# Optimization experiments

Hardware: AMD Instinct MI355X
Metric: run time of the kernel (lower is better)

## Reference

```python
import jax, jax.numpy as jnp
import numpy as np

N, DEG = 20000, 16
E = N * DEG
D_IN, D_HID, D_OUT, L = 1024, 512, 128, 3


def setup_inputs() -> dict:
    key = jax.random.key(0)
    ks = jax.random.split(key, 16)
    scale = 0.02
    X = jax.random.normal(ks[0], (N, D_IN), dtype=jnp.float32)
    senders = jax.random.randint(ks[1], (E,), 0, N)
    receivers = jnp.repeat(jnp.arange(N), DEG)  # sorted, every node has DEG neighbors
    inp = {"X": X, "senders": senders, "receivers": receivers}
    ki = 2
    for l in range(L):
        din = D_IN >> l
        dh = D_HID >> l
        inp[f"lw{l}"] = jax.random.normal(ks[ki], (2 * din, dh), jnp.float32) * scale; ki += 1
        inp[f"lb{l}"] = jnp.zeros((dh,), jnp.float32)
        inp[f"aw{l}"] = jax.random.normal(ks[ki], (din, dh), jnp.float32) * scale; ki += 1
        inp[f"aq{l}"] = jax.random.normal(ks[ki], (dh,), jnp.float32) * scale; ki += 1
    inp["ow"] = jax.random.normal(ks[ki], (D_HID >> (L - 1), D_OUT), jnp.float32) * scale
    inp["ob"] = jnp.zeros((D_OUT,), jnp.float32)
    return inp


def _attend(h, senders, receivers, aw, aq):
    # scores depend only on the neighbor (sender) embedding: q @ relu(W h_j)
    logits = jnp.einsum('nh,h->n', jax.nn.relu(h @ aw), aq)            # [N]
    el = logits[senders]                                               # [E]
    m = jax.ops.segment_max(el, receivers, num_segments=N)            # per-receiver max
    w = jnp.exp(el - m[receivers])                                     # [E]
    denom = jax.ops.segment_sum(w, receivers, num_segments=N)         # [N]
    msg = jax.ops.segment_sum(w[:, None] * h[senders], receivers, num_segments=N)  # [N,D]
    return msg / denom[:, None]


def reference(X, senders, receivers,
              lw0, lb0, aw0, aq0,
              lw1, lb1, aw1, aq1,
              lw2, lb2, aw2, aq2,
              ow, ob):
    params = [(lw0, lb0, aw0, aq0), (lw1, lb1, aw1, aq1), (lw2, lb2, aw2, aq2)]
    h = X
    for lw, lb, aw, aq in params:
        hN = _attend(h, senders, receivers, aw, aq)
        h = jax.nn.relu(jnp.concatenate([h, hN], axis=1) @ lw + lb)
    return h[14] @ ow + ob
```

## Files before the change

### kernel.cpp

```cpp
#include <hip/hip_runtime.h>
#include <math.h>

typedef unsigned short ushort_t;
typedef __attribute__((ext_vector_type(8))) short short8;
typedef __attribute__((ext_vector_type(4))) float f32x4;

#define NN    20000
#define DEG   16
constexpr int MAXL2 = 17;
constexpr int MAXL1 = 289;
constexpr int L0PAD = 73 * 64;

__device__ __forceinline__ ushort_t f2bf(float f) {
    unsigned u = __float_as_uint(f);
    return (ushort_t)((u + 0x7FFFu + ((u >> 16) & 1u)) >> 16);
}

__global__ __launch_bounds__(256)
void k_frontier(const int* __restrict__ senders,
                int* __restrict__ list2, int* __restrict__ inv2,
                int* __restrict__ list1, int* __restrict__ inv1,
                int* __restrict__ cnts,
                const float* __restrict__ aw0, ushort_t* __restrict__ awT,
                const float* __restrict__ aw1,
                const float* __restrict__ lw1, const float* __restrict__ aw2,
                const float* __restrict__ lw2, const float* __restrict__ ow,
                float* __restrict__ dummy,
                float4* __restrict__ zp, int n4, int nzb) {
    int t = threadIdx.x;
    int bb = (int)blockIdx.x;
    if (bb > 0) {
        int b = bb - 1;
        if (b < nzb) {
            int i = b * 256 + t;
            if (i < n4) zp[i] = make_float4(0.f, 0.f, 0.f, 0.f);
            return;
        }
        b -= nzb;
        if (b < 512) {
            __shared__ float tile[32][33];
            int bx = b & 15, by = b >> 4;
            int i0 = t >> 3, j0 = (t & 7) * 4;
            float4 v = *(const float4*)(aw0 + (size_t)(by * 32 + i0) * 512 + bx * 32 + j0);
            tile[i0][j0] = v.x; tile[i0][j0 + 1] = v.y; tile[i0][j0 + 2] = v.z; tile[i0][j0 + 3] = v.w;
            __syncthreads();
            int n = bx * 32 + i0, kc = j0;
            ushort4 o;
            o.x = f2bf(tile[kc][i0]);     o.y = f2bf(tile[kc + 1][i0]);
            o.z = f2bf(tile[kc + 2][i0]); o.w = f2bf(tile[kc + 3][i0]);
            *(ushort4*)(awT + (size_t)n * 1024 + by * 32 + kc) = o;
            return;
        }
        b -= 512;
        const float4* src; int base;
        if (b < 64)        { src = (const float4*)lw1; base = b * 1024; }
        else if (b < 96)   { src = (const float4*)aw1; base = (b - 64) * 1024; }
        else if (b < 104)  { src = (const float4*)aw2; base = (b - 96) * 1024; }
        else if (b < 120)  { src = (const float4*)lw2; base = (b - 104) * 1024; }
        else               { src = (const float4*)ow;  base = (b - 120) * 1024; }
        float s = 0.f;
#pragma unroll
        for (int i = 0; i < 4; i++) {
            float4 v = src[base + i * 256 + t];
            s += v.x + v.y + v.z + v.w;
        }
        if (s == 1234.5678f) dummy[0] = s;
        return;
    }
    __shared__ unsigned bm[625];
    __shared__ int cnt;
    __shared__ int lloc[MAXL2];
    auto clear = [&]() { for (int i = t; i < 625; i += 256) bm[i] = 0u; if (t == 0) cnt = 0; };
    clear(); __syncthreads();
    if (t < 17) {
        int node = (t < 16) ? senders[14 * DEG + t] : 14;
        unsigned bit = 1u << (node & 31);
        unsigned old = atomicOr(&bm[node >> 5], bit);
        if (!(old & bit)) { int p = atomicAdd(&cnt, 1); list2[p] = node; inv2[node] = p; lloc[p] = node; }
    }
    __syncthreads();
    int c2 = cnt;
    if (t == 0) cnts[2] = c2;
    __syncthreads(); clear(); __syncthreads();
    for (int i = t; i < c2 * 17; i += 256) {
        int r = i / 17, k = i - r * 17;
        int node = (k < 16) ? senders[lloc[r] * DEG + k] : lloc[r];
        unsigned bit = 1u << (node & 31);
        unsigned old = atomicOr(&bm[node >> 5], bit);
        if (!(old & bit)) { int p = atomicAdd(&cnt, 1); list1[p] = node; inv1[node] = p; }
    }
    __syncthreads();
    if (t == 0) { int c1 = cnt; cnts[1] = c1; cnts[0] = c1 * 16; }
}

__global__ __launch_bounds__(256)
void k_prep(const float* __restrict__ X, const int* __restrict__ senders,
            const int* __restrict__ list1, const int* __restrict__ cnts,
            ushort_t* __restrict__ Xg) {
    int r = blockIdx.x;
    int t = threadIdx.x;
    int rc = cnts[0];
    ushort4 o = make_ushort4(0, 0, 0, 0);
    if (r < rc) {
        int n = list1[r >> 4];
        int s = senders[n * DEG + (r & 15)];
        float4 v = *(const float4*)(X + (size_t)s * 1024 + t * 4);
        o.x = f2bf(v.x); o.y = f2bf(v.y); o.z = f2bf(v.z); o.w = f2bf(v.w);
    }
    *(ushort4*)(Xg + (size_t)r * 1024 + t * 4) = o;
}

__global__ __launch_bounds__(256)
void k_logits_mfma(const ushort_t* __restrict__ Xg,
                   const ushort_t* __restrict__ WT,
                   const float* __restrict__ aq, float* __restrict__ lgc,
                   const int* __restrict__ cnt) {
    __shared__ short As[64 * 40];
    __shared__ short Bs[64 * 40];
    int rcnt = *cnt;
    int row0 = blockIdx.x * 64;
    if (row0 >= rcnt) return;
    int col0 = blockIdx.y * 64;
    int t = threadIdx.x;
    int w = t >> 6, lane = t & 63;

    int sr = t >> 2, sk = (t & 3) * 8;
    const ushort_t* ap = Xg + (size_t)(row0 + sr) * 1024 + sk;
    const ushort_t* bp = WT + (size_t)(col0 + sr) * 1024 + sk;

    int fm = lane & 15, fq = lane >> 4;
    const short* arow = As + (w * 16 + fm) * 40 + fq * 8;
    const short* brow = Bs + fm * 40 + fq * 8;

    f32x4 acc0 = {0.f,0.f,0.f,0.f}, acc1 = {0.f,0.f,0.f,0.f};
    f32x4 acc2 = {0.f,0.f,0.f,0.f}, acc3 = {0.f,0.f,0.f,0.f};

    short8 pa = *(const short8*)(ap);
    short8 pb = *(const short8*)(bp);
    for (int k0 = 0; k0 < 1024; k0 += 32) {
        *(short8*)(As + sr * 40 + sk) = pa;
        *(short8*)(Bs + sr * 40 + sk) = pb;
        __syncthreads();
        if (k0 + 32 < 1024) {
            pa = *(const short8*)(ap + k0 + 32);
            pb = *(const short8*)(bp + k0 + 32);
        }
        short8 af = *(const short8*)arow;
        short8 b0 = *(const short8*)(brow);
        short8 b1 = *(const short8*)(brow + 16 * 40);
        short8 b2 = *(const short8*)(brow + 32 * 40);
        short8 b3 = *(const short8*)(brow + 48 * 40);
        acc0 = __builtin_amdgcn_mfma_f32_16x16x32_bf16(af, b0, acc0, 0, 0, 0);
        acc1 = __builtin_amdgcn_mfma_f32_16x16x32_bf16(af, b1, acc1, 0, 0, 0);
        acc2 = __builtin_amdgcn_mfma_f32_16x16x32_bf16(af, b2, acc2, 0, 0, 0);
        acc3 = __builtin_amdgcn_mfma_f32_16x16x32_bf16(af, b3, acc3, 0, 0, 0);
        __syncthreads();
    }

    float aqv0 = aq[col0 + fm],      aqv1 = aq[col0 + 16 + fm];
    float aqv2 = aq[col0 + 32 + fm], aqv3 = aq[col0 + 48 + fm];
#pragma unroll
    for (int r = 0; r < 4; r++) {
        float v = fmaxf(acc0[r], 0.f) * aqv0 + fmaxf(acc1[r], 0.f) * aqv1
                + fmaxf(acc2[r], 0.f) * aqv2 + fmaxf(acc3[r], 0.f) * aqv3;
#pragma unroll
        for (int off = 1; off < 16; off <<= 1) v += __shfl_xor(v, off);
        if (fm == 0) atomicAdd(&lgc[row0 + w * 16 + fq * 4 + r], v);
    }
}

__global__ __launch_bounds__(256)
void k_agg0(const float* __restrict__ X, const float* __restrict__ lgc0,
            const int* __restrict__ senders, const int* __restrict__ list1,
            const int* __restrict__ cnt1, float* __restrict__ hN0) {
    __shared__ int   s_row[DEG];
    __shared__ float s_w[DEG];
    __shared__ float s_sc;
    int b = blockIdx.x;
    if (b >= *cnt1) return;
    int t = threadIdx.x;
    if (t < DEG) {
        s_row[t] = senders[list1[b] * DEG + t];
        s_w[t]   = lgc0[b * DEG + t];
    }
    __syncthreads();
    if (t == 0) {
        float m = -1e30f;
        for (int k = 0; k < DEG; k++) m = fmaxf(m, s_w[k]);
        float d = 0.f;
        for (int k = 0; k < DEG; k++) { float w = __expf(s_w[k] - m); s_w[k] = w; d += w; }
        s_sc = 1.f / d;
    }
    __syncthreads();
    float scale = s_sc;
    int dI = t * 4;
    float4 acc = make_float4(0.f, 0.f, 0.f, 0.f);
#pragma unroll
    for (int k = 0; k < DEG; k++) {
        float w = s_w[k];
        float4 v = *(const float4*)(X + (size_t)s_row[k] * 1024 + dI);
        acc.x += w * v.x; acc.y += w * v.y; acc.z += w * v.z; acc.w += w * v.w;
    }
    acc.x *= scale; acc.y *= scale; acc.z *= scale; acc.w *= scale;
    *(float4*)(hN0 + (size_t)b * 1024 + dI) = acc;
}

__global__ __launch_bounds__(256)
void k_mm0(const float* __restrict__ X, const float* __restrict__ hN0,
           const int* __restrict__ list1, const float* __restrict__ B,
           float* __restrict__ C0p, const int* __restrict__ cnt) {
    __shared__ float As[32][68];
    __shared__ float Bs[32][64];
    int rcnt = *cnt;
    int row0 = blockIdx.x * 64;
    if (row0 >= rcnt) return;
    int col0 = blockIdx.y * 64;
    int kbeg = blockIdx.z * 128;
    int t = threadIdx.x;
    int ty = t >> 4, tx = t & 15;
    int lr = t >> 2, kaoff = (t & 3) * 4;
    int grow = row0 + lr;
    bool rowValid = grow < rcnt;
    const float* rp;
    if (kbeg < 1024) rp = rowValid ? X + (size_t)list1[grow] * 1024 + kbeg : X;
    else             rp = rowValid ? hN0 + (size_t)grow * 1024 + (kbeg - 1024) : hN0;
    const float* Bp = B + (size_t)kbeg * 512 + col0;
    int bidx0 = t, bidx1 = t + 256;

    auto loadA = [&](int k) -> float4 {
        if (!rowValid) return make_float4(0.f, 0.f, 0.f, 0.f);
        return *(const float4*)(rp + k);
    };
    auto loadB = [&](int idx, int k0) -> float4 {
        int row = idx >> 4, c4 = (idx & 15) * 4;
        return *(const float4*)(Bp + (size_t)(k0 + row) * 512 + c4);
    };

    float4 pa0 = loadA(kaoff);
    float4 pa1 = loadA(kaoff + 16);
    float4 pb0 = loadB(bidx0, 0);
    float4 pb1 = loadB(bidx1, 0);

    float acc[4][4] = {};
    for (int k0 = 0; k0 < 128; k0 += 32) {
        As[kaoff + 0][lr] = pa0.x; As[kaoff + 1][lr] = pa0.y;
        As[kaoff + 2][lr] = pa0.z; As[kaoff + 3][lr] = pa0.w;
        As[kaoff + 16][lr] = pa1.x; As[kaoff + 17][lr] = pa1.y;
        As[kaoff + 18][lr] = pa1.z; As[kaoff + 19][lr] = pa1.w;
        *(float4*)&Bs[bidx0 >> 4][(bidx0 & 15) * 4] = pb0;
        *(float4*)&Bs[bidx1 >> 4][(bidx1 & 15) * 4] = pb1;
        __syncthreads();
        if (k0 + 32 < 128) {
            pa0 = loadA(k0 + 32 + kaoff);
            pa1 = loadA(k0 + 32 + kaoff + 16);
            pb0 = loadB(bidx0, k0 + 32);
            pb1 = loadB(bidx1, k0 + 32);
        }
#pragma unroll
        for (int kk = 0; kk < 32; kk++) {
            float4 a4 = *(const float4*)&As[kk][ty * 4];
            float4 b4 = *(const float4*)&Bs[kk][tx * 4];
            float a[4] = {a4.x, a4.y, a4.z, a4.w};
            float b[4] = {b4.x, b4.y, b4.z, b4.w};
#pragma unroll
            for (int i = 0; i < 4; i++)
#pragma unroll
                for (int j = 0; j < 4; j++) acc[i][j] += a[i] * b[j];
        }
        __syncthreads();
    }
#pragma unroll
    for (int i = 0; i < 4; i++) {
        int r = row0 + ty * 4 + i;
        if (r < rcnt) {
            float* Crow = C0p + ((size_t)blockIdx.z * MAXL1 + r) * 512 + col0 + tx * 4;
            *(float4*)Crow = make_float4(acc[i][0], acc[i][1], acc[i][2], acc[i][3]);
        }
    }
}

__global__ __launch_bounds__(256)
void k_bias_logits(const float* __restrict__ C0p, const float* __restrict__ lb0,
                   const float* __restrict__ aw1, const float* __restrict__ aq1,
                   float* __restrict__ h1, float* __restrict__ lgc1,
                   const int* __restrict__ cnt) {
    __shared__ float sh[512];
    __shared__ float red[4];
    int r = blockIdx.x;
    if (r >= *cnt) return;
    int t = threadIdx.x;
    float v0 = lb0[t], v1 = lb0[256 + t];
    const float* base = C0p + (size_t)r * 512;
#pragma unroll
    for (int z = 0; z < 16; z++) {
        v0 += base[(size_t)z * MAXL1 * 512 + t];
        v1 += base[(size_t)z * MAXL1 * 512 + 256 + t];
    }
    v0 = v0 > 0.f ? v0 : 0.f;
    v1 = v1 > 0.f ? v1 : 0.f;
    sh[t] = v0; sh[256 + t] = v1;
    h1[(size_t)r * 512 + t] = v0;
    h1[(size_t)r * 512 + 256 + t] = v1;
    __syncthreads();
    float dot = 0.f;
    for (int k = 0; k < 512; k += 4) {
        dot += sh[k + 0] * aw1[(size_t)(k + 0) * 256 + t]
             + sh[k + 1] * aw1[(size_t)(k + 1) * 256 + t]
             + sh[k + 2] * aw1[(size_t)(k + 2) * 256 + t]
             + sh[k + 3] * aw1[(size_t)(k + 3) * 256 + t];
    }
    float v = (dot > 0.f ? dot : 0.f) * aq1[t];
#pragma unroll
    for (int off = 1; off < 64; off <<= 1) v += __shfl_xor(v, off);
    if ((t & 63) == 0) red[t >> 6] = v;
    __syncthreads();
    if (t == 0) lgc1[r] = red[0] + red[1] + red[2] + red[3];
}

__global__ __launch_bounds__(256)
void k_tail1(const float* __restrict__ h1, const float* __restrict__ lgc1,
             const int* __restrict__ senders, const int* __restrict__ list2,
             const int* __restrict__ inv1, const int* __restrict__ cnts,
             const float* __restrict__ lw1, const float* __restrict__ lb1,
             float* __restrict__ h2) {
    __shared__ __align__(16) float As[17][1024];
    __shared__ float sw[17][16];
    __shared__ int   srow[17][16];
    __shared__ int   orow[17];
    __shared__ float psum[16][17 * 16];
    int c2 = cnts[2];
    int t = threadIdx.x;
    int b = blockIdx.x;

    for (int i = t; i < c2 * 16; i += 256) {
        int j = i >> 4, k = i & 15;
        int s = senders[list2[j] * DEG + k];
        int rr = inv1[s];
        srow[j][k] = rr;
        sw[j][k] = lgc1[rr];
    }
    if (t < c2) orow[t] = inv1[list2[t]];
    __syncthreads();
    if (t < c2) {
        float m = -1e30f;
        for (int k = 0; k < 16; k++) m = fmaxf(m, sw[t][k]);
        float d = 0.f;
        for (int k = 0; k < 16; k++) { float w = __expf(sw[t][k] - m); sw[t][k] = w; d += w; }
        float inv = 1.f / d;
        for (int k = 0; k < 16; k++) sw[t][k] *= inv;
    }
    __syncthreads();
    for (int e = t; e < c2 * 128; e += 256) {
        int j = e >> 7, d4 = (e & 127) * 4;
        *(float4*)&As[j][d4] = *(const float4*)&h1[(size_t)orow[j] * 512 + d4];
        float4 a = make_float4(0.f, 0.f, 0.f, 0.f);
#pragma unroll
        for (int k = 0; k < 16; k++) {
            float w = sw[j][k];
            float4 v = *(const float4*)&h1[(size_t)srow[j][k] * 512 + d4];
            a.x += w * v.x; a.y += w * v.y; a.z += w * v.z; a.w += w * v.w;
        }
        *(float4*)&As[j][512 + d4] = a;
    }
    __syncthreads();
    int c = t & 15, s = t >> 4;
    int gc = b * 16 + c;
    float acc[17];
#pragma unroll
    for (int j = 0; j < 17; j++) acc[j] = 0.f;
    for (int k = s * 64; k < s * 64 + 64; k += 4) {
        float b0 = lw1[(size_t)(k + 0) * 256 + gc];
        float b1 = lw1[(size_t)(k + 1) * 256 + gc];
        float b2 = lw1[(size_t)(k + 2) * 256 + gc];
        float b3 = lw1[(size_t)(k + 3) * 256 + gc];
#pragma unroll
        for (int j = 0; j < 17; j++) {
            float4 a = *(const float4*)&As[j][k];
            acc[j] += a.x * b0 + a.y * b1 + a.z * b2 + a.w * b3;
        }
    }
#pragma unroll
    for (int j = 0; j < 17; j++) psum[s][j * 16 + c] = acc[j];
    __syncthreads();
    for (int e = t; e < c2 * 16; e += 256) {
        int j = e >> 4, cc = e & 15;
        float v = 0.f;
#pragma unroll
        for (int s2 = 0; s2 < 16; s2++) v += psum[s2][j * 16 + cc];
        v += lb1[b * 16 + cc];
        h2[(size_t)j * 256 + b * 16 + cc] = v > 0.f ? v : 0.f;
    }
}

__global__ __launch_bounds__(512)
void k_tail2(const float* __restrict__ h2, const int* __restrict__ senders,
             const int* __restrict__ inv2, const int* __restrict__ cnts,
             const float* __restrict__ aw2, const float* __restrict__ aq2,
             const float* __restrict__ lw2, const float* __restrict__ lb2,
             const float* __restrict__ ow, const float* __restrict__ ob,
             float* __restrict__ out) {
    __shared__ __align__(16) float sh2[17][256];
    __shared__ __align__(16) float psum[8][17][128];
    __shared__ __align__(16) float h3in[512];
    __shared__ __align__(16) float sh3[128];
    __shared__ __align__(16) float psumB[16][128];
    __shared__ float slog[17];
    __shared__ float swt[16];
    __shared__ int   srow2[16];
    __shared__ int   srow14;
    int c2 = cnts[2];
    int t = threadIdx.x;
    for (int e = t; e < c2 * 64; e += 512) {
        int j = e >> 6, d4 = (e & 63) * 4;
        *(float4*)&sh2[j][d4] = *(const float4*)&h2[(size_t)j * 256 + d4];
    }
    if (t < c2) slog[t] = 0.f;
    if (t < 16) srow2[t] = inv2[senders[14 * DEG + t]];
    if (t == 31) srow14 = inv2[14];
    __syncthreads();
    {
        int cg = t & 31;
        int s  = (t >> 5) & 7;
        int jg = t >> 8;
        int j0 = jg * 9;
        int jend = min(c2, j0 + 9);
        float4 acc[9];
#pragma unroll
        for (int i = 0; i < 9; i++) acc[i] = make_float4(0.f, 0.f, 0.f, 0.f);
        const float* ap = aw2 + cg * 4;
        for (int k = s * 32; k < s * 32 + 32; k++) {
            float4 bv = *(const float4*)(ap + (size_t)k * 128);
#pragma unroll
            for (int i = 0; i < 9; i++) {
                int j = j0 + i;
                if (j < jend) {
                    float a = sh2[j][k];
                    acc[i].x += a * bv.x; acc[i].y += a * bv.y;
                    acc[i].z += a * bv.z; acc[i].w += a * bv.w;
                }
            }
        }
#pragma unroll
        for (int i = 0; i < 9; i++) {
            int j = j0 + i;
            if (j < jend) *(float4*)&psum[s][j][cg * 4] = acc[i];
        }
    }
    __syncthreads();
    for (int e = t; e < c2 * 128; e += 512) {
        int j = e >> 7, c = e & 127;
        float v = 0.f;
#pragma unroll
        for (int s = 0; s < 8; s++) v += psum[s][j][c];
        v = v > 0.f ? v : 0.f;
        atomicAdd(&slog[j], v * aq2[c]);
    }
    __syncthreads();
    if (t == 0) {
        float m = -1e30f;
        for (int k = 0; k < 16; k++) m = fmaxf(m, slog[srow2[k]]);
        float d = 0.f;
        for (int k = 0; k < 16; k++) { float w = __expf(slog[srow2[k]] - m); swt[k] = w; d += w; }
        float inv = 1.f / d;
        for (int k = 0; k < 16; k++) swt[k] *= inv;
    }
    __syncthreads();
    if (t < 256) {
        float a = 0.f;
#pragma unroll
        for (int k = 0; k < 16; k++) a += swt[k] * sh2[srow2[k]][t];
        h3in[256 + t] = a;
    } else {
        int d = t - 256;
        h3in[d] = sh2[srow14][d];
    }
    __syncthreads();
    {
        int cg = t & 31, s = t >> 5;
        float4 acc = make_float4(0.f, 0.f, 0.f, 0.f);
        const float* bp = lw2 + cg * 4;
        for (int k = s * 32; k < s * 32 + 32; k++) {
            float4 bv = *(const float4*)(bp + (size_t)k * 128);
            float a = h3in[k];
            acc.x += a * bv.x; acc.y += a * bv.y; acc.z += a * bv.z; acc.w += a * bv.w;
        }
        *(float4*)&psumB[s][cg * 4] = acc;
    }
    __syncthreads();
    if (t < 128) {
        float v = lb2[t];
#pragma unroll
        for (int s = 0; s < 16; s++) v += psumB[s][t];
        sh3[t] = v > 0.f ? v : 0.f;
    }
    __syncthreads();
    {
        int cg = t & 31, s = t >> 5;
        float4 acc = make_float4(0.f, 0.f, 0.f, 0.f);
        const float* bp = ow + cg * 4;
        for (int k = s * 8; k < s * 8 + 8; k++) {
            float4 bv = *(const float4*)(bp + (size_t)k * 128);
            float a = sh3[k];
            acc.x += a * bv.x; acc.y += a * bv.y; acc.z += a * bv.z; acc.w += a * bv.w;
        }
        *(float4*)&psumB[s][cg * 4] = acc;
    }
    __syncthreads();
    if (t < 128) {
        float v = ob[t];
#pragma unroll
        for (int s = 0; s < 16; s++) v += psumB[s][t];
        out[t] = v;
    }
}

extern "C" void kernel_launch(void* const* d_in, const int* in_sizes, int n_in,
                              void* d_out, int out_size, void* d_ws, size_t ws_size,
                              hipStream_t stream) {
    const float* X       = (const float*)d_in[0];
    const int*   senders = (const int*)d_in[1];
    const float* lw0 = (const float*)d_in[3];
    const float* lb0 = (const float*)d_in[4];
    const float* aw0 = (const float*)d_in[5];
    const float* aq0 = (const float*)d_in[6];
    const float* lw1 = (const float*)d_in[7];
    const float* lb1 = (const float*)d_in[8];
    const float* aw1 = (const float*)d_in[9];
    const float* aq1 = (const float*)d_in[10];
    const float* lw2 = (const float*)d_in[11];
    const float* lb2 = (const float*)d_in[12];
    const float* aw2 = (const float*)d_in[13];
    const float* aq2 = (const float*)d_in[14];
    const float* owp = (const float*)d_in[15];
    const float* obp = (const float*)d_in[16];
    float* out = (float*)d_out;

    char* ws = (char*)d_ws;
    size_t off = 0;
    auto alloc = [&](size_t nbytes) -> void* {
        void* p = ws + off;
        off += (nbytes + 255) & ~(size_t)255;
        return p;
    };
    float* lgc0 = (float*)alloc(L0PAD * 4);
    size_t zero_end = off;
    float* lgc1 = (float*)alloc(MAXL1 * 4);
    int* inv1  = (int*)alloc(NN * 4);
    int* inv2  = (int*)alloc(NN * 4);
    int* list1 = (int*)alloc(MAXL1 * 4);
    int* list2 = (int*)alloc(MAXL2 * 4);
    int* cnts  = (int*)alloc(16);
    float* dummy = (float*)alloc(16);
    ushort_t* Xg  = (ushort_t*)alloc((size_t)L0PAD * 1024 * 2);
    ushort_t* awT = (ushort_t*)alloc((size_t)512 * 1024 * 2);
    float* C0p  = (float*)alloc((size_t)16 * MAXL1 * 512 * 4);
    float* hN0c = (float*)alloc((size_t)MAXL1 * 1024 * 4);
    float* h1c  = (float*)alloc((size_t)MAXL1 * 512 * 4);
    float* h2c  = (float*)alloc((size_t)MAXL2 * 256 * 4);
    (void)in_sizes; (void)n_in; (void)out_size; (void)ws_size;

    int nz4 = (int)(zero_end / 16);
    int nzb = (nz4 + 255) / 256;

    hipLaunchKernelGGL(k_frontier, dim3(1 + nzb + 512 + 124), dim3(256), 0, stream,
                       senders, list2, inv2, list1, inv1, cnts,
                       aw0, awT, aw1, lw1, aw2, lw2, owp, dummy,
                       (float4*)ws, nz4, nzb);
    hipLaunchKernelGGL(k_prep, dim3(L0PAD), dim3(256), 0, stream,
                       X, senders, list1, cnts, Xg);
    hipLaunchKernelGGL(k_logits_mfma, dim3(73, 8), dim3(256), 0, stream,
                       Xg, awT, aq0, lgc0, cnts + 0);
    hipLaunchKernelGGL(k_agg0, dim3(MAXL1), dim3(256), 0, stream,
                       X, lgc0, senders, list1, cnts + 1, hN0c);
    hipLaunchKernelGGL(k_mm0, dim3(5, 8, 16), dim3(256), 0, stream,
                       X, hN0c, list1, lw0, C0p, cnts + 1);
    hipLaunchKernelGGL(k_bias_logits, dim3(MAXL1), dim3(256), 0, stream,
                       C0p, lb0, aw1, aq1, h1c, lgc1, cnts + 1);
    hipLaunchKernelGGL(k_tail1, dim3(16), dim3(256), 0, stream,
                       h1c, lgc1, senders, list2, inv1, cnts, lw1, lb1, h2c);
    hipLaunchKernelGGL(k_tail2, dim3(1), dim3(512), 0, stream,
                       h2c, senders, inv2, cnts, aw2, aq2, lw2, lb2, owp, obp, out);
}
```

Before: 246.9 us.

## Fuse layer-0 aggregation into logits kernel and drop frontier deduplication

The layer-0 softmax aggregation kernel is folded into the MFMA logits kernel. A per-row-panel atomic counter lets the last of the 8 column blocks for a panel run aggregation for its 4 nodes, which removes one kernel launch. The layer-1 frontier is no longer deduplicated with a bitmap. It now lists every sender slot directly (c2*17 entries), so duplicate nodes get recomputed and inv1 is overwritten by the last writer. This skips a sync and the atomics, but the redundant rows add extra work downstream and the ordering of inv1 changes.

```diff
diff --git a/kernel.cpp b/kernel.cpp
--- a/kernel.cpp
+++ b/kernel.cpp
@@ -70,8 +70,9 @@
     __shared__ unsigned bm[625];
     __shared__ int cnt;
     __shared__ int lloc[MAXL2];
-    auto clear = [&]() { for (int i = t; i < 625; i += 256) bm[i] = 0u; if (t == 0) cnt = 0; };
-    clear(); __syncthreads();
+    for (int i = t; i < 625; i += 256) bm[i] = 0u;
+    if (t == 0) cnt = 0;
+    __syncthreads();
     if (t < 17) {
         int node = (t < 16) ? senders[14 * DEG + t] : 14;
         unsigned bit = 1u << (node & 31);
@@ -80,17 +81,13 @@
     }
     __syncthreads();
     int c2 = cnt;
-    if (t == 0) cnts[2] = c2;
-    __syncthreads(); clear(); __syncthreads();
+    if (t == 0) { cnts[2] = c2; cnts[1] = c2 * 17; cnts[0] = c2 * 17 * 16; }
     for (int i = t; i < c2 * 17; i += 256) {
         int r = i / 17, k = i - r * 17;
         int node = (k < 16) ? senders[lloc[r] * DEG + k] : lloc[r];
-        unsigned bit = 1u << (node & 31);
-        unsigned old = atomicOr(&bm[node >> 5], bit);
-        if (!(old & bit)) { int p = atomicAdd(&cnt, 1); list1[p] = node; inv1[node] = p; }
-    }
-    __syncthreads();
-    if (t == 0) { int c1 = cnt; cnts[1] = c1; cnts[0] = c1 * 16; }
+        list1[i] = node;
+        inv1[node] = i;
+    }
 }
 
 __global__ __launch_bounds__(256)
@@ -114,9 +111,16 @@
 void k_logits_mfma(const ushort_t* __restrict__ Xg,
                    const ushort_t* __restrict__ WT,
                    const float* __restrict__ aq, float* __restrict__ lgc,
-                   const int* __restrict__ cnt) {
+                   const int* __restrict__ cnt,
+                   const float* __restrict__ X, const int* __restrict__ senders,
+                   const int* __restrict__ list1, int* __restrict__ panel_done,
+                   float* __restrict__ hN0) {
     __shared__ short As[64 * 40];
     __shared__ short Bs[64 * 40];
+    __shared__ int   s_old;
+    __shared__ float sw[16];
+    __shared__ int   srow[16];
+    __shared__ float s_sc;
     int rcnt = *cnt;
     int row0 = blockIdx.x * 64;
     if (row0 >= rcnt) return;
@@ -167,42 +171,45 @@
         for (int off = 1; off < 16; off <<= 1) v += __shfl_xor(v, off);
         if (fm == 0) atomicAdd(&lgc[row0 + w * 16 + fq * 4 + r], v);
     }
-}
-
-__global__ __launch_bounds__(256)
-void k_agg0(const float* __restrict__ X, const float* __restrict__ lgc0,
-            const int* __restrict__ senders, const int* __restrict__ list1,
-            const int* __restrict__ cnt1, float* __restrict__ hN0) {
-    __shared__ int   s_row[DEG];
-    __shared__ float s_w[DEG];
-    __shared__ float s_sc;
-    int b = blockIdx.x;
-    if (b >= *cnt1) return;
-    int t = threadIdx.x;
-    if (t < DEG) {
-        s_row[t] = senders[list1[b] * DEG + t];
-        s_w[t]   = lgc0[b * DEG + t];
-    }
+
     __syncthreads();
     if (t == 0) {
-        float m = -1e30f;
-        for (int k = 0; k < DEG; k++) m = fmaxf(m, s_w[k]);
-        float d = 0.f;
-        for (int k = 0; k < DEG; k++) { float w = __expf(s_w[k] - m); s_w[k] = w; d += w; }
-        s_sc = 1.f / d;
-    }
-    __syncthreads();
-    float scale = s_sc;
-    int dI = t * 4;
-    float4 acc = make_float4(0.f, 0.f, 0.f, 0.f);
-#pragma unroll
-    for (int k = 0; k < DEG; k++) {
-        float w = s_w[k];
-        float4 v = *(const float4*)(X + (size_t)s_row[k] * 1024 + dI);
-        acc.x += w * v.x; acc.y += w * v.y; acc.z += w * v.z; acc.w += w * v.w;
-    }
-    acc.x *= scale; acc.y *= scale; acc.z *= scale; acc.w *= scale;
-    *(float4*)(hN0 + (size_t)b * 1024 + dI) = acc;
+        __threadfence();
+        s_old = atomicAdd(&panel_done[blockIdx.x], 1);
+    }
+    __syncthreads();
+    if (s_old != 7) return;
+    __threadfence();
+    int bx = blockIdx.x;
+    for (int rr = 0; rr < 4; rr++) {
+        int b = bx * 4 + rr;
+        if (b * 16 >= rcnt) break;
+        if (t < 16) {
+            sw[t]   = lgc[b * DEG + t];
+            srow[t] = senders[list1[b] * DEG + t];
+        }
+        __syncthreads();
+        if (t == 0) {
+            float m = -1e30f;
+            for (int k = 0; k < DEG; k++) m = fmaxf(m, sw[k]);
+            float d = 0.f;
+            for (int k = 0; k < DEG; k++) { float wv = __expf(sw[k] - m); sw[k] = wv; d += wv; }
+            s_sc = 1.f / d;
+        }
+        __syncthreads();
+        float scale = s_sc;
+        int dI = t * 4;
+        float4 acc = make_float4(0.f, 0.f, 0.f, 0.f);
+#pragma unroll
+        for (int k = 0; k < DEG; k++) {
+            float wv = sw[k];
+            float4 v = *(const float4*)(X + (size_t)srow[k] * 1024 + dI);
+            acc.x += wv * v.x; acc.y += wv * v.y; acc.z += wv * v.z; acc.w += wv * v.w;
+        }
+        acc.x *= scale; acc.y *= scale; acc.z *= scale; acc.w *= scale;
+        *(float4*)(hN0 + (size_t)b * 1024 + dI) = acc;
+        __syncthreads();
+    }
 }
 
 __global__ __launch_bounds__(256)
@@ -543,6 +550,7 @@
         return p;
     };
     float* lgc0 = (float*)alloc(L0PAD * 4);
+    int* panel_done = (int*)alloc(73 * 4);
     size_t zero_end = off;
     float* lgc1 = (float*)alloc(MAXL1 * 4);
     int* inv1  = (int*)alloc(NN * 4);
@@ -569,9 +577,8 @@
     hipLaunchKernelGGL(k_prep, dim3(L0PAD), dim3(256), 0, stream,
                        X, senders, list1, cnts, Xg);
     hipLaunchKernelGGL(k_logits_mfma, dim3(73, 8), dim3(256), 0, stream,
-                       Xg, awT, aq0, lgc0, cnts + 0);
-    hipLaunchKernelGGL(k_agg0, dim3(MAXL1), dim3(256), 0, stream,
-                       X, lgc0, senders, list1, cnts + 1, hN0c);
+                       Xg, awT, aq0, lgc0, cnts + 0,
+                       X, senders, list1, panel_done, hN0c);
     hipLaunchKernelGGL(k_mm0, dim3(5, 8, 16), dim3(256), 0, stream,
                        X, hN0c, list1, lw0, C0p, cnts + 1);
     hipLaunchKernelGGL(k_bias_logits, dim3(MAXL1), dim3(256), 0, stream,
```

New measurement: 270.5 us. +9.6%, slower.
